# Kernel optimization log

Hardware: AMD Instinct MI355X
Metric: run time of the kernel (lower is better)

Reference implementation:

```python
import jax, jax.numpy as jnp
import numpy as np

LAYERS = 3
DILATION = 2
RES_NORM = 1.0 / np.sqrt(2.0).astype(np.float32)
NEG_SLOPE = 0.2
T, B, D = 256, 128, 1024


def setup_inputs() -> dict:
    key = jax.random.key(0)
    k0, k1, k2, k3, k4 = jax.random.split(key, 5)
    s = 1.0 / np.sqrt(D)  # torch GRUCell default init bound
    x = jax.random.normal(k0, (1, T, B, D), dtype=jnp.float32)
    W_ih = jax.random.uniform(k1, (LAYERS, 3 * D, D), jnp.float32, -s, s)
    W_hh = jax.random.uniform(k2, (LAYERS, 3 * D, D), jnp.float32, -s, s)
    b_ih = jax.random.uniform(k3, (LAYERS, 3 * D), jnp.float32, -s, s)
    b_hh = jax.random.uniform(k4, (LAYERS, 3 * D), jnp.float32, -s, s)
    return {"x": x, "W_ih": W_ih, "W_hh": W_hh, "b_ih": b_ih, "b_hh": b_hh}


def _gru_cell(x, h, W_ih, W_hh, b_ih, b_hh):
    # torch.nn.GRUCell math
    gi = x @ W_ih.T + b_ih  # [B, 3D]
    gh = h @ W_hh.T + b_hh  # [B, 3D]
    i_r, i_z, i_n = jnp.split(gi, 3, axis=-1)
    h_r, h_z, h_n = jnp.split(gh, 3, axis=-1)
    r = jax.nn.sigmoid(i_r + h_r)
    z = jax.nn.sigmoid(i_z + h_z)
    n = jnp.tanh(i_n + r * h_n)
    return (1.0 - z) * n + z * h


def reference(x, W_ih, W_hh, b_ih, b_hh):
    xs = x[0]  # squeeze(0) -> [T, B, D]
    b, d = xs.shape[1], xs.shape[2]
    # dilated hidden buffers: layer l keeps DILATION**l past hiddens (init None -> zeros)
    bufs0 = tuple(jnp.zeros((DILATION ** l, b, d), xs.dtype) for l in range(LAYERS))

    def step(bufs, x_t):
        h_in = x_t
        new_bufs = []
        for l in range(LAYERS):
            h_out = _gru_cell(h_in, bufs[l][0], W_ih[l], W_hh[l], b_ih[l], b_hh[l])
            # append h_out, pop oldest (roll buffer)
            new_bufs.append(jnp.concatenate([bufs[l][1:], h_out[None]], axis=0))
            # layers > 1 -> dilated residual + LeakyReLU(0.2), scaled by 1/sqrt(2)
            h_in = jax.nn.leaky_relu((h_out + h_in) * RES_NORM, negative_slope=NEG_SLOPE)
        return tuple(new_bufs), h_in

    _, outs = jax.lax.scan(step, bufs0, xs)  # outs: [T, B, D]
    return outs[None]  # unsqueeze(0) -> [1, T, B, D]
```

## Files before the change

### kernel.cpp

```cpp
#include <hip/hip_runtime.h>
#include <hip/hip_bf16.h>

#define TT 256
#define D 1024
#define BD (128 * 1024)
#define NWPL 85
#define NWG 256
#define NUSED 255
#define STEPS (TT + 2)
#define ROWLEN 1040

typedef __attribute__((ext_vector_type(8))) short bf16x8;
typedef __attribute__((ext_vector_type(4))) float f32x4;

__device__ __forceinline__ unsigned short f2bf(float f) {
    __hip_bfloat16 h = __float2bfloat16(f);
    return *reinterpret_cast<unsigned short*>(&h);
}
__device__ __forceinline__ float bf2f(unsigned short u) {
    unsigned v = (unsigned)u << 16;
    return __builtin_bit_cast(float, v);
}

__global__ __launch_bounds__(256) void cvt_f32_bf16(const float* __restrict__ in,
                                                    unsigned short* __restrict__ out, int n) {
    int i = (blockIdx.x * 256 + threadIdx.x) * 8;
    if (i + 8 <= n) {
        float4 a = *(const float4*)(in + i);
        float4 b = *(const float4*)(in + i + 4);
        unsigned short t[8] = { f2bf(a.x), f2bf(a.y), f2bf(a.z), f2bf(a.w),
                                f2bf(b.x), f2bf(b.y), f2bf(b.z), f2bf(b.w) };
        *(uint4*)(out + i) = *(const uint4*)t;
    }
}

__device__ __forceinline__ void gbar(unsigned* __restrict__ bar, int grp) {
    __syncthreads();
    if (threadIdx.x == 0) {
        unsigned* xcnt = bar + grp * 32;
        unsigned* mcnt = bar + 256;
        unsigned* gen  = bar + 288;
        __builtin_amdgcn_fence(__ATOMIC_RELEASE, "agent");
        unsigned g = __hip_atomic_load(gen, __ATOMIC_RELAXED, __HIP_MEMORY_SCOPE_AGENT);
        unsigned a = __hip_atomic_fetch_add(xcnt, 1u, __ATOMIC_RELAXED, __HIP_MEMORY_SCOPE_AGENT);
        if (a == 31u) {
            __hip_atomic_store(xcnt, 0u, __ATOMIC_RELAXED, __HIP_MEMORY_SCOPE_AGENT);
            unsigned m = __hip_atomic_fetch_add(mcnt, 1u, __ATOMIC_ACQ_REL, __HIP_MEMORY_SCOPE_AGENT);
            if (m == 7u) {
                __hip_atomic_store(mcnt, 0u, __ATOMIC_RELAXED, __HIP_MEMORY_SCOPE_AGENT);
                __hip_atomic_store(gen, g + 1u, __ATOMIC_RELEASE, __HIP_MEMORY_SCOPE_AGENT);
            }
        }
        while (__hip_atomic_load(gen, __ATOMIC_RELAXED, __HIP_MEMORY_SCOPE_AGENT) == g)
            __builtin_amdgcn_s_sleep(1);
        __builtin_amdgcn_fence(__ATOMIC_ACQUIRE, "agent");
    }
    __syncthreads();
}

__global__ __launch_bounds__(256, 1) void dgru_persistent(
    const unsigned short* __restrict__ xbf,
    const float* __restrict__ Wih, const float* __restrict__ Whh,
    const float* __restrict__ bih, const float* __restrict__ bhh,
    unsigned short* __restrict__ ring_bf, float* __restrict__ ring_f,
    unsigned short* __restrict__ hin_bf,
    float* __restrict__ out,
    unsigned* __restrict__ bar)
{
    __shared__ unsigned short wlds[78 * ROWLEN];

    const int grp = blockIdx.x & 7;
    const int p = 32 * grp + (blockIdx.x >> 3);
    if (p >= NUSED) {
        for (int s = 0; s < STEPS; ++s) gbar(bar, grp);
        return;
    }
    const int layer = p / NWPL;
    const int u     = p % NWPL;
    const int ncols = (u < 4) ? 13 : 12;
    const int c0    = u * 12 + (u < 4 ? u : 4);

    {
        const float* w0 = Wih + (size_t)layer * 3 * D * D;
        const float* w1 = Whh + (size_t)layer * 3 * D * D;
        const int nrows = 6 * ncols;
        for (int rid = 0; rid < nrows; ++rid) {
            int m   = rid / (3 * ncols);
            int rem = rid - m * 3 * ncols;
            int g   = rem / ncols;
            int c   = rem - g * ncols;
            const float* src = (m ? w1 : w0) + ((size_t)g * D + c0 + c) * D + threadIdx.x * 4;
            float4 v = *(const float4*)src;
            ushort4 o = { f2bf(v.x), f2bf(v.y), f2bf(v.z), f2bf(v.w) };
            *(ushort4*)&wlds[rid * ROWLEN + threadIdx.x * 4] = o;
        }
        __syncthreads();
    }

    const int tid  = threadIdx.x;
    const int wave = tid >> 6;
    const int lane = tid & 63;
    const int r15  = lane & 15;
    const int kq   = lane >> 4;
    const int kq8  = kq * 8;
    const int c_cl = (r15 < ncols) ? r15 : (ncols - 1);
    const bool cvalid = r15 < ncols;
    const int col  = c0 + c_cl;

    const float bi2 = bih[layer * 3 * D + 2 * D + col];
    const float bh0 = bhh[layer * 3 * D + col];
    const float bh1 = bhh[layer * 3 * D + D + col];
    const float bh2 = bhh[layer * 3 * D + 2 * D + col];
    const float bs0 = bih[layer * 3 * D + col] + bh0;
    const float bs1 = bih[layer * 3 * D + D + col] + bh1;

    const unsigned short* bp[6];
    #pragma unroll
    for (int mg = 0; mg < 6; ++mg) bp[mg] = wlds + (mg * ncols + c_cl) * ROWLEN;

    const int arow_off0 = (wave * 32 + r15) * D;
    const int arow_off1 = (wave * 32 + 16 + r15) * D;

    const int R  = (layer == 0) ? 2 : (layer == 1 ? 3 : 5);
    const int rb = (layer == 0) ? 0 : (layer == 1 ? 2 : 5);

    for (int s = 0; s < STEPS; ++s) {
        const int t = s - layer;
        if (t >= 0 && t < TT) {
            const unsigned short* hinb = layer ? hin_bf + (size_t)((layer - 1) * 2 + (t & 1)) * BD
                                               : xbf + (size_t)t * BD;
            const int rs = (t + 1) % R, wsl = t % R;
            const unsigned short* hprevb = ring_bf + (size_t)(rb + rs) * BD;
            const float*  hprevf = ring_f + (size_t)(rb + rs) * BD;
            float*        houtf  = ring_f + (size_t)(rb + wsl) * BD;
            unsigned short* houtb = ring_bf + (size_t)(rb + wsl) * BD;

            float hpv[8], rsv[8];
            #pragma unroll
            for (int rtl = 0; rtl < 2; ++rtl)
                #pragma unroll
                for (int q = 0; q < 4; ++q) {
                    const int row = wave * 32 + rtl * 16 + kq * 4 + q;
                    const size_t idx = (size_t)row * D + col;
                    hpv[rtl * 4 + q] = hprevf[idx];
                    rsv[rtl * 4 + q] = bf2f(hinb[idx]);
                }

            f32x4 acc[2][2][3] = {};
            bf16x8 A0[16], A1[16], A2[16];

#define ISSUE1(Av, KS, SL) { \
            Av[(SL) * 4 + 0] = *(const bf16x8*)(hinb   + arow_off0 + (KS) * 32 + kq8); \
            Av[(SL) * 4 + 1] = *(const bf16x8*)(hprevb + arow_off0 + (KS) * 32 + kq8); \
            Av[(SL) * 4 + 2] = *(const bf16x8*)(hinb   + arow_off1 + (KS) * 32 + kq8); \
            Av[(SL) * 4 + 3] = *(const bf16x8*)(hprevb + arow_off1 + (KS) * 32 + kq8); }
#define ISSUEG(Av, BASE) { ISSUE1(Av, (BASE) + 0, 0) ISSUE1(Av, (BASE) + 1, 1) \
                           ISSUE1(Av, (BASE) + 2, 2) ISSUE1(Av, (BASE) + 3, 3) \
                           __builtin_amdgcn_sched_barrier(0); }
#define COMPG(Av, BASE) { _Pragma("unroll") for (int kk = 0; kk < 4; ++kk) { \
            bf16x8 Bv[6]; \
            _Pragma("unroll") for (int mg = 0; mg < 6; ++mg) \
                Bv[mg] = *(const bf16x8*)(bp[mg] + ((BASE) + kk) * 32 + kq8); \
            _Pragma("unroll") for (int g = 0; g < 3; ++g) { \
                acc[0][0][g] = __builtin_amdgcn_mfma_f32_16x16x32_bf16(Av[kk * 4 + 0], Bv[g],     acc[0][0][g], 0, 0, 0); \
                acc[0][1][g] = __builtin_amdgcn_mfma_f32_16x16x32_bf16(Av[kk * 4 + 1], Bv[3 + g], acc[0][1][g], 0, 0, 0); \
                acc[1][0][g] = __builtin_amdgcn_mfma_f32_16x16x32_bf16(Av[kk * 4 + 2], Bv[g],     acc[1][0][g], 0, 0, 0); \
                acc[1][1][g] = __builtin_amdgcn_mfma_f32_16x16x32_bf16(Av[kk * 4 + 3], Bv[3 + g], acc[1][1][g], 0, 0, 0); } } \
            __builtin_amdgcn_sched_barrier(0); }

            ISSUEG(A0, 0);  ISSUEG(A1, 4);  ISSUEG(A2, 8);
            COMPG(A0, 0);   ISSUEG(A0, 12);
            COMPG(A1, 4);   ISSUEG(A1, 16);
            COMPG(A2, 8);   ISSUEG(A2, 20);
            COMPG(A0, 12);  ISSUEG(A0, 24);
            COMPG(A1, 16);  ISSUEG(A1, 28);
            COMPG(A2, 20);
            COMPG(A0, 24);
            COMPG(A1, 28);

            #pragma unroll
            for (int rtl = 0; rtl < 2; ++rtl) {
                #pragma unroll
                for (int q = 0; q < 4; ++q) {
                    const int row = wave * 32 + rtl * 16 + kq * 4 + q;
                    const size_t idx = (size_t)row * D + col;
                    float xr = acc[rtl][0][0][q] + acc[rtl][1][0][q] + bs0;
                    float xz = acc[rtl][0][1][q] + acc[rtl][1][1][q] + bs1;
                    float rg = 1.f / (1.f + __expf(-xr));
                    float zg = 1.f / (1.f + __expf(-xz));
                    float ng = tanhf(acc[rtl][0][2][q] + bi2 + rg * (acc[rtl][1][2][q] + bh2));
                    float hp = hpv[rtl * 4 + q];
                    float h  = (1.f - zg) * ng + zg * hp;
                    float v = (h + rsv[rtl * 4 + q]) * 0.70710678f;
                    float y = v > 0.f ? v : 0.2f * v;
                    if (cvalid) {
                        __hip_atomic_store(&houtf[idx], h, __ATOMIC_RELAXED, __HIP_MEMORY_SCOPE_AGENT);
                        __hip_atomic_store(&houtb[idx], f2bf(h), __ATOMIC_RELAXED, __HIP_MEMORY_SCOPE_AGENT);
                        if (layer == 2) {
                            __hip_atomic_store(&out[(size_t)t * BD + idx], y, __ATOMIC_RELAXED, __HIP_MEMORY_SCOPE_AGENT);
                        } else {
                            __hip_atomic_store(&hin_bf[(size_t)(layer * 2 + (t & 1)) * BD + idx],
                                               f2bf(y), __ATOMIC_RELAXED, __HIP_MEMORY_SCOPE_AGENT);
                        }
                    }
                }
            }
        }
        gbar(bar, grp);
    }
}

extern "C" void kernel_launch(void* const* d_in, const int* in_sizes, int n_in,
                              void* d_out, int out_size, void* d_ws, size_t ws_size,
                              hipStream_t stream) {
    const float* x   = (const float*)d_in[0];
    const float* Wih = (const float*)d_in[1];
    const float* Whh = (const float*)d_in[2];
    const float* bih = (const float*)d_in[3];
    const float* bhh = (const float*)d_in[4];
    float* out = (float*)d_out;

    char* ws = (char*)d_ws;
    size_t off = 0;
    auto alloc = [&](size_t bytes) -> void* {
        void* p = ws + off;
        off += (bytes + 255) & ~(size_t)255;
        return p;
    };

    const int NX = TT * BD;
    unsigned short* xbf = (unsigned short*)alloc((size_t)NX * 2);

    size_t zstart = off;
    unsigned short* ring_bf = (unsigned short*)alloc((size_t)10 * BD * 2);
    float*          ring_f  = (float*)alloc((size_t)10 * BD * 4);
    unsigned short* hin_bf  = (unsigned short*)alloc((size_t)4 * BD * 2);
    unsigned*       bar     = (unsigned*)alloc(2048);
    size_t zbytes = off - zstart;

    cvt_f32_bf16<<<NX / 8 / 256, 256, 0, stream>>>(x, xbf, NX);
    hipMemsetAsync(ws + zstart, 0, zbytes, stream);

    dgru_persistent<<<NWG, 256, 0, stream>>>(
        xbf, Wih, Whh, bih, bhh,
        ring_bf, ring_f, hin_bf, out,
        bar);
}
```

Before: 5.819 ms.

## Replace global per-step barrier with per-layer progress-flag dataflow synchronization

Removes the grid-wide barrier run every step. Each workgroup now publishes a monotonically increasing progress counter, and wave 0 polls only the counters of the producer and consumer layers it depends on. The hidden-state and inter-layer rings are enlarged (to 2/4/8 and 8 slots) so layers can run several timesteps apart without overwriting data still being read. The LDS row padding is also changed. The trade-off is more polling traffic and ring memory, plus correctness that now depends on getting the threshold logic exactly right.

```diff
diff --git a/kernel.cpp b/kernel.cpp
--- a/kernel.cpp
+++ b/kernel.cpp
@@ -7,8 +7,7 @@
 #define NWPL 85
 #define NWG 256
 #define NUSED 255
-#define STEPS (TT + 2)
-#define ROWLEN 1040
+#define ROWLEN 1048
 
 typedef __attribute__((ext_vector_type(8))) short bf16x8;
 typedef __attribute__((ext_vector_type(4))) float f32x4;
@@ -34,47 +33,20 @@
     }
 }
 
-__device__ __forceinline__ void gbar(unsigned* __restrict__ bar, int grp) {
-    __syncthreads();
-    if (threadIdx.x == 0) {
-        unsigned* xcnt = bar + grp * 32;
-        unsigned* mcnt = bar + 256;
-        unsigned* gen  = bar + 288;
-        __builtin_amdgcn_fence(__ATOMIC_RELEASE, "agent");
-        unsigned g = __hip_atomic_load(gen, __ATOMIC_RELAXED, __HIP_MEMORY_SCOPE_AGENT);
-        unsigned a = __hip_atomic_fetch_add(xcnt, 1u, __ATOMIC_RELAXED, __HIP_MEMORY_SCOPE_AGENT);
-        if (a == 31u) {
-            __hip_atomic_store(xcnt, 0u, __ATOMIC_RELAXED, __HIP_MEMORY_SCOPE_AGENT);
-            unsigned m = __hip_atomic_fetch_add(mcnt, 1u, __ATOMIC_ACQ_REL, __HIP_MEMORY_SCOPE_AGENT);
-            if (m == 7u) {
-                __hip_atomic_store(mcnt, 0u, __ATOMIC_RELAXED, __HIP_MEMORY_SCOPE_AGENT);
-                __hip_atomic_store(gen, g + 1u, __ATOMIC_RELEASE, __HIP_MEMORY_SCOPE_AGENT);
-            }
-        }
-        while (__hip_atomic_load(gen, __ATOMIC_RELAXED, __HIP_MEMORY_SCOPE_AGENT) == g)
-            __builtin_amdgcn_s_sleep(1);
-        __builtin_amdgcn_fence(__ATOMIC_ACQUIRE, "agent");
-    }
-    __syncthreads();
-}
-
-__global__ __launch_bounds__(256, 1) void dgru_persistent(
+__global__ __launch_bounds__(256, 1) void dgru_dataflow(
     const unsigned short* __restrict__ xbf,
     const float* __restrict__ Wih, const float* __restrict__ Whh,
     const float* __restrict__ bih, const float* __restrict__ bhh,
     unsigned short* __restrict__ ring_bf, float* __restrict__ ring_f,
-    unsigned short* __restrict__ hin_bf,
+    unsigned short* __restrict__ hin_ring,
     float* __restrict__ out,
-    unsigned* __restrict__ bar)
+    unsigned* __restrict__ prog)
 {
     __shared__ unsigned short wlds[78 * ROWLEN];
 
     const int grp = blockIdx.x & 7;
     const int p = 32 * grp + (blockIdx.x >> 3);
-    if (p >= NUSED) {
-        for (int s = 0; s < STEPS; ++s) gbar(bar, grp);
-        return;
-    }
+    if (p >= NUSED) return;
     const int layer = p / NWPL;
     const int u     = p % NWPL;
     const int ncols = (u < 4) ? 13 : 12;
@@ -108,11 +80,9 @@
     const int col  = c0 + c_cl;
 
     const float bi2 = bih[layer * 3 * D + 2 * D + col];
-    const float bh0 = bhh[layer * 3 * D + col];
-    const float bh1 = bhh[layer * 3 * D + D + col];
     const float bh2 = bhh[layer * 3 * D + 2 * D + col];
-    const float bs0 = bih[layer * 3 * D + col] + bh0;
-    const float bs1 = bih[layer * 3 * D + D + col] + bh1;
+    const float bs0 = bih[layer * 3 * D + col] + bhh[layer * 3 * D + col];
+    const float bs1 = bih[layer * 3 * D + D + col] + bhh[layer * 3 * D + D + col];
 
     const unsigned short* bp[6];
     #pragma unroll
@@ -121,92 +91,128 @@
     const int arow_off0 = (wave * 32 + r15) * D;
     const int arow_off1 = (wave * 32 + 16 + r15) * D;
 
-    const int R  = (layer == 0) ? 2 : (layer == 1 ? 3 : 5);
-    const int rb = (layer == 0) ? 0 : (layer == 1 ? 2 : 5);
-
-    for (int s = 0; s < STEPS; ++s) {
-        const int t = s - layer;
-        if (t >= 0 && t < TT) {
-            const unsigned short* hinb = layer ? hin_bf + (size_t)((layer - 1) * 2 + (t & 1)) * BD
-                                               : xbf + (size_t)t * BD;
-            const int rs = (t + 1) % R, wsl = t % R;
-            const unsigned short* hprevb = ring_bf + (size_t)(rb + rs) * BD;
-            const float*  hprevf = ring_f + (size_t)(rb + rs) * BD;
-            float*        houtf  = ring_f + (size_t)(rb + wsl) * BD;
-            unsigned short* houtb = ring_bf + (size_t)(rb + wsl) * BD;
-
-            float hpv[8], rsv[8];
+    const int dil = 1 << layer;
+    const int R   = 2 << layer;
+    const int rb  = (layer == 0) ? 0 : (layer == 1 ? 2 : 6);
+
+    unsigned* pr0 = prog;
+    unsigned* pr1 = prog + 128;
+    unsigned* pr2 = prog + 256;
+    unsigned* myflag = prog + layer * 128 + u;
+
+    unsigned *a1, *a2, *a3;
+    if (layer == 0)      { a1 = pr0; a2 = pr1; a3 = pr2; }
+    else if (layer == 1) { a1 = pr0; a2 = pr1; a3 = pr2; }
+    else                 { a1 = pr1; a2 = pr2; a3 = pr2; }
+
+    const int j2 = (lane < 21) ? lane + 64 : lane;
+
+    for (int t = 0; t < TT; ++t) {
+        int th1, th2, th3;
+        if (layer == 0)      { th1 = t;     th2 = t - 7; th3 = 0; }
+        else if (layer == 1) { th1 = t + 1; th2 = t - 1; th3 = t - 7; }
+        else                 { th1 = t + 1; th2 = t - 3; th3 = 0; }
+
+        if (wave == 0) {
+            for (;;) {
+                bool ok = true;
+                if (th1 > 0) ok = ok && (int)__hip_atomic_load(a1 + lane, __ATOMIC_RELAXED, __HIP_MEMORY_SCOPE_AGENT) >= th1
+                                     && (int)__hip_atomic_load(a1 + j2,   __ATOMIC_RELAXED, __HIP_MEMORY_SCOPE_AGENT) >= th1;
+                if (th2 > 0) ok = ok && (int)__hip_atomic_load(a2 + lane, __ATOMIC_RELAXED, __HIP_MEMORY_SCOPE_AGENT) >= th2
+                                     && (int)__hip_atomic_load(a2 + j2,   __ATOMIC_RELAXED, __HIP_MEMORY_SCOPE_AGENT) >= th2;
+                if (th3 > 0) ok = ok && (int)__hip_atomic_load(a3 + lane, __ATOMIC_RELAXED, __HIP_MEMORY_SCOPE_AGENT) >= th3
+                                     && (int)__hip_atomic_load(a3 + j2,   __ATOMIC_RELAXED, __HIP_MEMORY_SCOPE_AGENT) >= th3;
+                if (__all(ok)) break;
+                __builtin_amdgcn_s_sleep(1);
+            }
+            __builtin_amdgcn_fence(__ATOMIC_ACQUIRE, "agent");
+        }
+        __syncthreads();
+
+        const unsigned short* hinb = layer ? hin_ring + (size_t)((layer - 1) * 8 + (t & 7)) * BD
+                                           : xbf + (size_t)t * BD;
+        const int rs = (t + dil) % R, wsl = t % R;
+        const unsigned short* hprevb = ring_bf + (size_t)(rb + rs) * BD;
+        const float*  hprevf = ring_f + (size_t)(rb + rs) * BD;
+        float*        houtf  = ring_f + (size_t)(rb + wsl) * BD;
+        unsigned short* houtb = ring_bf + (size_t)(rb + wsl) * BD;
+
+        float hpv[8], rsv[8];
+        #pragma unroll
+        for (int rtl = 0; rtl < 2; ++rtl)
             #pragma unroll
-            for (int rtl = 0; rtl < 2; ++rtl)
-                #pragma unroll
-                for (int q = 0; q < 4; ++q) {
-                    const int row = wave * 32 + rtl * 16 + kq * 4 + q;
-                    const size_t idx = (size_t)row * D + col;
-                    hpv[rtl * 4 + q] = hprevf[idx];
-                    rsv[rtl * 4 + q] = bf2f(hinb[idx]);
-                }
-
-            f32x4 acc[2][2][3] = {};
-            bf16x8 A0[16], A1[16], A2[16];
+            for (int q = 0; q < 4; ++q) {
+                const int row = wave * 32 + rtl * 16 + kq * 4 + q;
+                const size_t idx = (size_t)row * D + col;
+                hpv[rtl * 4 + q] = hprevf[idx];
+                rsv[rtl * 4 + q] = bf2f(hinb[idx]);
+            }
+
+        f32x4 acc[2][2][3] = {};
+        bf16x8 A0[16], A1[16], A2[16];
 
 #define ISSUE1(Av, KS, SL) { \
-            Av[(SL) * 4 + 0] = *(const bf16x8*)(hinb   + arow_off0 + (KS) * 32 + kq8); \
-            Av[(SL) * 4 + 1] = *(const bf16x8*)(hprevb + arow_off0 + (KS) * 32 + kq8); \
-            Av[(SL) * 4 + 2] = *(const bf16x8*)(hinb   + arow_off1 + (KS) * 32 + kq8); \
-            Av[(SL) * 4 + 3] = *(const bf16x8*)(hprevb + arow_off1 + (KS) * 32 + kq8); }
+        Av[(SL) * 4 + 0] = *(const bf16x8*)(hinb   + arow_off0 + (KS) * 32 + kq8); \
+        Av[(SL) * 4 + 1] = *(const bf16x8*)(hprevb + arow_off0 + (KS) * 32 + kq8); \
+        Av[(SL) * 4 + 2] = *(const bf16x8*)(hinb   + arow_off1 + (KS) * 32 + kq8); \
+        Av[(SL) * 4 + 3] = *(const bf16x8*)(hprevb + arow_off1 + (KS) * 32 + kq8); }
 #define ISSUEG(Av, BASE) { ISSUE1(Av, (BASE) + 0, 0) ISSUE1(Av, (BASE) + 1, 1) \
                            ISSUE1(Av, (BASE) + 2, 2) ISSUE1(Av, (BASE) + 3, 3) \
                            __builtin_amdgcn_sched_barrier(0); }
 #define COMPG(Av, BASE) { _Pragma("unroll") for (int kk = 0; kk < 4; ++kk) { \
-            bf16x8 Bv[6]; \
-            _Pragma("unroll") for (int mg = 0; mg < 6; ++mg) \
-                Bv[mg] = *(const bf16x8*)(bp[mg] + ((BASE) + kk) * 32 + kq8); \
-            _Pragma("unroll") for (int g = 0; g < 3; ++g) { \
-                acc[0][0][g] = __builtin_amdgcn_mfma_f32_16x16x32_bf16(Av[kk * 4 + 0], Bv[g],     acc[0][0][g], 0, 0, 0); \
-                acc[0][1][g] = __builtin_amdgcn_mfma_f32_16x16x32_bf16(Av[kk * 4 + 1], Bv[3 + g], acc[0][1][g], 0, 0, 0); \
-                acc[1][0][g] = __builtin_amdgcn_mfma_f32_16x16x32_bf16(Av[kk * 4 + 2], Bv[g],     acc[1][0][g], 0, 0, 0); \
-                acc[1][1][g] = __builtin_amdgcn_mfma_f32_16x16x32_bf16(Av[kk * 4 + 3], Bv[3 + g], acc[1][1][g], 0, 0, 0); } } \
-            __builtin_amdgcn_sched_barrier(0); }
-
-            ISSUEG(A0, 0);  ISSUEG(A1, 4);  ISSUEG(A2, 8);
-            COMPG(A0, 0);   ISSUEG(A0, 12);
-            COMPG(A1, 4);   ISSUEG(A1, 16);
-            COMPG(A2, 8);   ISSUEG(A2, 20);
-            COMPG(A0, 12);  ISSUEG(A0, 24);
-            COMPG(A1, 16);  ISSUEG(A1, 28);
-            COMPG(A2, 20);
-            COMPG(A0, 24);
-            COMPG(A1, 28);
-
+        bf16x8 Bv[6]; \
+        _Pragma("unroll") for (int mg = 0; mg < 6; ++mg) \
+            Bv[mg] = *(const bf16x8*)(bp[mg] + ((BASE) + kk) * 32 + kq8); \
+        _Pragma("unroll") for (int g = 0; g < 3; ++g) { \
+            acc[0][0][g] = __builtin_amdgcn_mfma_f32_16x16x32_bf16(Av[kk * 4 + 0], Bv[g],     acc[0][0][g], 0, 0, 0); \
+            acc[0][1][g] = __builtin_amdgcn_mfma_f32_16x16x32_bf16(Av[kk * 4 + 1], Bv[3 + g], acc[0][1][g], 0, 0, 0); \
+            acc[1][0][g] = __builtin_amdgcn_mfma_f32_16x16x32_bf16(Av[kk * 4 + 2], Bv[g],     acc[1][0][g], 0, 0, 0); \
+            acc[1][1][g] = __builtin_amdgcn_mfma_f32_16x16x32_bf16(Av[kk * 4 + 3], Bv[3 + g], acc[1][1][g], 0, 0, 0); } } \
+        __builtin_amdgcn_sched_barrier(0); }
+
+        ISSUEG(A0, 0);  ISSUEG(A1, 4);  ISSUEG(A2, 8);
+        COMPG(A0, 0);   ISSUEG(A0, 12);
+        COMPG(A1, 4);   ISSUEG(A1, 16);
+        COMPG(A2, 8);   ISSUEG(A2, 20);
+        COMPG(A0, 12);  ISSUEG(A0, 24);
+        COMPG(A1, 16);  ISSUEG(A1, 28);
+        COMPG(A2, 20);
+        COMPG(A0, 24);
+        COMPG(A1, 28);
+
+        #pragma unroll
+        for (int rtl = 0; rtl < 2; ++rtl) {
             #pragma unroll
-            for (int rtl = 0; rtl < 2; ++rtl) {
-                #pragma unroll
-                for (int q = 0; q < 4; ++q) {
-                    const int row = wave * 32 + rtl * 16 + kq * 4 + q;
-                    const size_t idx = (size_t)row * D + col;
-                    float xr = acc[rtl][0][0][q] + acc[rtl][1][0][q] + bs0;
-                    float xz = acc[rtl][0][1][q] + acc[rtl][1][1][q] + bs1;
-                    float rg = 1.f / (1.f + __expf(-xr));
-                    float zg = 1.f / (1.f + __expf(-xz));
-                    float ng = tanhf(acc[rtl][0][2][q] + bi2 + rg * (acc[rtl][1][2][q] + bh2));
-                    float hp = hpv[rtl * 4 + q];
-                    float h  = (1.f - zg) * ng + zg * hp;
-                    float v = (h + rsv[rtl * 4 + q]) * 0.70710678f;
-                    float y = v > 0.f ? v : 0.2f * v;
-                    if (cvalid) {
-                        __hip_atomic_store(&houtf[idx], h, __ATOMIC_RELAXED, __HIP_MEMORY_SCOPE_AGENT);
-                        __hip_atomic_store(&houtb[idx], f2bf(h), __ATOMIC_RELAXED, __HIP_MEMORY_SCOPE_AGENT);
-                        if (layer == 2) {
-                            __hip_atomic_store(&out[(size_t)t * BD + idx], y, __ATOMIC_RELAXED, __HIP_MEMORY_SCOPE_AGENT);
-                        } else {
-                            __hip_atomic_store(&hin_bf[(size_t)(layer * 2 + (t & 1)) * BD + idx],
-                                               f2bf(y), __ATOMIC_RELAXED, __HIP_MEMORY_SCOPE_AGENT);
-                        }
+            for (int q = 0; q < 4; ++q) {
+                const int row = wave * 32 + rtl * 16 + kq * 4 + q;
+                const size_t idx = (size_t)row * D + col;
+                float xr = acc[rtl][0][0][q] + acc[rtl][1][0][q] + bs0;
+                float xz = acc[rtl][0][1][q] + acc[rtl][1][1][q] + bs1;
+                float rg = 1.f / (1.f + __expf(-xr));
+                float zg = 1.f / (1.f + __expf(-xz));
+                float ng = tanhf(acc[rtl][0][2][q] + bi2 + rg * (acc[rtl][1][2][q] + bh2));
+                float hp = hpv[rtl * 4 + q];
+                float h  = (1.f - zg) * ng + zg * hp;
+                float v = (h + rsv[rtl * 4 + q]) * 0.70710678f;
+                float y = v > 0.f ? v : 0.2f * v;
+                if (cvalid) {
+                    __hip_atomic_store(&houtf[idx], h, __ATOMIC_RELAXED, __HIP_MEMORY_SCOPE_AGENT);
+                    __hip_atomic_store(&houtb[idx], f2bf(h), __ATOMIC_RELAXED, __HIP_MEMORY_SCOPE_AGENT);
+                    if (layer == 2) {
+                        __hip_atomic_store(&out[(size_t)t * BD + idx], y, __ATOMIC_RELAXED, __HIP_MEMORY_SCOPE_AGENT);
+                    } else {
+                        __hip_atomic_store(&hin_ring[(size_t)(layer * 8 + (t & 7)) * BD + idx],
+                                           f2bf(y), __ATOMIC_RELAXED, __HIP_MEMORY_SCOPE_AGENT);
                     }
                 }
             }
         }
-        gbar(bar, grp);
+
+        __syncthreads();
+        if (tid == 0) {
+            __builtin_amdgcn_fence(__ATOMIC_RELEASE, "agent");
+            __hip_atomic_store(myflag, (unsigned)(t + 1), __ATOMIC_RELAXED, __HIP_MEMORY_SCOPE_AGENT);
+        }
     }
 }
 
@@ -232,17 +238,17 @@
     unsigned short* xbf = (unsigned short*)alloc((size_t)NX * 2);
 
     size_t zstart = off;
-    unsigned short* ring_bf = (unsigned short*)alloc((size_t)10 * BD * 2);
-    float*          ring_f  = (float*)alloc((size_t)10 * BD * 4);
-    unsigned short* hin_bf  = (unsigned short*)alloc((size_t)4 * BD * 2);
-    unsigned*       bar     = (unsigned*)alloc(2048);
+    unsigned short* ring_bf  = (unsigned short*)alloc((size_t)14 * BD * 2);
+    float*          ring_f   = (float*)alloc((size_t)14 * BD * 4);
+    unsigned short* hin_ring = (unsigned short*)alloc((size_t)16 * BD * 2);
+    unsigned*       prog     = (unsigned*)alloc(2048);
     size_t zbytes = off - zstart;
 
     cvt_f32_bf16<<<NX / 8 / 256, 256, 0, stream>>>(x, xbf, NX);
     hipMemsetAsync(ws + zstart, 0, zbytes, stream);
 
-    dgru_persistent<<<NWG, 256, 0, stream>>>(
+    dgru_dataflow<<<NWG, 256, 0, stream>>>(
         xbf, Wih, Whh, bih, bhh,
-        ring_bf, ring_f, hin_bf, out,
-        bar);
-}
+        ring_bf, ring_f, hin_ring, out,
+        prog);
+}
```

New measurement: 6.001 ms. +3.1%, slower.
